# Kernel optimization log

Measured on AMD Instinct MI355X. Metric: run time of the kernel, lower is better.

## Reference

```python
import jax, jax.numpy as jnp
import numpy as np
import math

B, T, C, H = 4, 2048, 1024, 16
D = C // H  # head dim = 64

def setup_inputs() -> dict:
    key = jax.random.key(0)
    k1, k2, k3 = jax.random.split(key, 3)
    scale = 0.02
    return {
        "x": jax.random.normal(k1, (B, T, C), dtype=jnp.float32),
        "W_qkv": jax.random.normal(k2, (C, 3 * C), dtype=jnp.float32) * scale,
        "b_qkv": jnp.zeros((3 * C,), dtype=jnp.float32),
        "W_proj": jax.random.normal(k3, (C, C), dtype=jnp.float32) * scale,
        "b_proj": jnp.zeros((C,), dtype=jnp.float32),
    }

def reference(x, W_qkv, b_qkv, W_proj, b_proj):
    Bx, Tx, Cx = x.shape
    qkv = x @ W_qkv + b_qkv                      # [B, T, 3C]
    q, k, v = jnp.split(qkv, 3, axis=-1)
    # [B, T, C] -> [B, H, T, D]
    q = q.reshape(Bx, Tx, H, D).transpose(0, 2, 1, 3)
    k = k.reshape(Bx, Tx, H, D).transpose(0, 2, 1, 3)
    v = v.reshape(Bx, Tx, H, D).transpose(0, 2, 1, 3)
    scores = jnp.einsum("bhqd,bhkd->bhqk", q, k) * (1.0 / math.sqrt(D))
    causal = jnp.tril(jnp.ones((Tx, Tx), dtype=bool))  # [T, T]
    scores = jnp.where(causal[None, None, :, :], scores, jnp.finfo(scores.dtype).min)
    attn = jax.nn.softmax(scores, axis=-1)
    # dropout(p=0.1) in the original is stochastic; omitted for a deterministic baseline
    out = jnp.einsum("bhqk,bhkd->bhqd", attn, v)   # [B, H, T, D]
    out = out.transpose(0, 2, 1, 3).reshape(Bx, Tx, Cx)
    return out @ W_proj + b_proj
```

## Files before the change

kernel.cpp:

```cpp
#include <hip/hip_runtime.h>
#include <hip/hip_bf16.h>
#include <cstdint>
#include <cstddef>

#define Bsz 4
#define Tseq 2048
#define Cdim 1024
#define Hh 16
#define Dh 64

typedef unsigned short u16;
typedef __bf16 bfx8 __attribute__((ext_vector_type(8)));
typedef float f32x4 __attribute__((ext_vector_type(4)));
typedef float f32x16 __attribute__((ext_vector_type(16)));
typedef unsigned short u16x8 __attribute__((ext_vector_type(8)));

#define AS1 __attribute__((address_space(1)))
#define AS3 __attribute__((address_space(3)))

#define QSCALE 0.18033688f

__device__ __forceinline__ u16 f2b(float f) {
  union { float f; unsigned u; } x; x.f = f;
  unsigned r = x.u + 0x7FFFu + ((x.u >> 16) & 1u);
  return (u16)(r >> 16);
}
__device__ __forceinline__ float b2f(u16 b) {
  union { unsigned u; float f; } x; x.u = ((unsigned)b) << 16; return x.f;
}
__device__ __forceinline__ unsigned cvtpk(float lo, float hi) {
  unsigned r;
  asm("v_cvt_pk_bf16_f32 %0, %1, %2" : "=v"(r) : "v"(lo), "v"(hi));
  return r;
}
__device__ __forceinline__ void swap32(unsigned &a, unsigned &b) {
  asm("v_permlane32_swap_b32 %0, %1" : "+v"(a), "+v"(b));
}

__global__ __launch_bounds__(256) void cvt_f32_bf16(const float* __restrict__ in,
                                                    u16* __restrict__ out, int n4) {
  int i = blockIdx.x * 256 + threadIdx.x;
  if (i < n4) {
    const float4 v = reinterpret_cast<const float4*>(in)[i];
    ushort4 o;
    o.x = f2b(v.x); o.y = f2b(v.y); o.z = f2b(v.z); o.w = f2b(v.w);
    reinterpret_cast<ushort4*>(out)[i] = o;
  }
}

__global__ __launch_bounds__(256) void transpose_cvt(const float* __restrict__ in,
                                                     u16* __restrict__ out, int R, int Cn) {
  __shared__ float tile[32][33];
  const int c0 = blockIdx.x * 32, r0 = blockIdx.y * 32;
  const int tx = threadIdx.x, ty = threadIdx.y;
  for (int i = ty; i < 32; i += 8)
    tile[i][tx] = in[(size_t)(r0 + i) * Cn + c0 + tx];
  __syncthreads();
  for (int i = ty; i < 32; i += 8)
    out[(size_t)(c0 + i) * R + r0 + tx] = f2b(tile[tx][i]);
}

template<int MODE>
__global__ __launch_bounds__(512, 4) void gemm_bt(const u16* __restrict__ A, const u16* __restrict__ Bt,
                                                  const float* __restrict__ bias, void* __restrict__ Cout,
                                                  u16* __restrict__ vtout,
                                                  int M, int N, int K) {
  __shared__ __align__(16) u16 Alds[3][4096];
  __shared__ __align__(16) u16 Blds[3][8192];
  const int tid = threadIdx.x;
  const int lane = tid & 63;
  const int wid = tid >> 6;
  const int nwgx = gridDim.x;
  const int nwg = nwgx * gridDim.y;
  int lin = blockIdx.y * nwgx + blockIdx.x;
  lin = (lin & 7) * (nwg >> 3) + (lin >> 3);
  const int mbase = (lin / nwgx) * 128;
  const int nbase = (lin % nwgx) * 256;
  const int wm = wid & 1, wn = wid >> 1;

  const int sLlow = lane >> 3;
  const int s8 = (lane & 7) ^ sLlow;
  const int srow = 2 * (wid * 8 + sLlow) + (s8 >> 2);
  const int skof = (s8 & 3) * 8;

  const u16* pa  = A  + (size_t)(mbase + srow) * K + skof;
  const u16* pb0 = Bt + (size_t)(nbase + srow) * K + skof;
  const u16* pb1 = pb0 + (size_t)128 * K;

  const int raA = wm * 64 + (lane & 15);
  const int LA = raA >> 1;
  const int pA = ((raA & 1) * 4 + (lane >> 4)) ^ (LA & 7);
  const int aoffw = LA * 64 + pA * 8;
  const int rbB = wn * 64 + (lane & 15);
  const int LB = rbB >> 1;
  const int pB = ((rbB & 1) * 4 + (lane >> 4)) ^ (LB & 7);
  const int boffw = LB * 64 + pB * 8;

  AS3 u16* aldsb = (AS3 u16*)&Alds[0][0];
  AS3 u16* bldsb = (AS3 u16*)&Blds[0][0];

  const f32x4 vzero = {0.f, 0.f, 0.f, 0.f};
  f32x4 acc[4][4];
  #pragma unroll
  for (int i = 0; i < 4; ++i)
    #pragma unroll
    for (int j = 0; j < 4; ++j) acc[i][j] = vzero;

  const int NT = K >> 5;

  auto stage = [&](int slot) {
    __builtin_amdgcn_global_load_lds((AS1 void*)const_cast<u16*>(pa),
                                     (AS3 void*)&Alds[slot][wid * 512], 16, 0, 0);
    __builtin_amdgcn_global_load_lds((AS1 void*)const_cast<u16*>(pb0),
                                     (AS3 void*)&Blds[slot][wid * 512], 16, 0, 0);
    __builtin_amdgcn_global_load_lds((AS1 void*)const_cast<u16*>(pb1),
                                     (AS3 void*)&Blds[slot][4096 + wid * 512], 16, 0, 0);
    pa += 32; pb0 += 32; pb1 += 32;
  };

  stage(0);
  stage(1);
  asm volatile("s_waitcnt vmcnt(3)" ::: "memory");
  __builtin_amdgcn_s_barrier();

  int slot = 0, pf = 2;
  for (int t = 0; t < NT; ++t) {
    if (t + 2 < NT) stage(pf);

    bfx8 af[4], bfv[4];
    {
      AS3 u16* ap = aldsb + slot * 4096 + aoffw;
      AS3 u16* bp = bldsb + slot * 8192 + boffw;
      asm volatile("ds_read_b128 %0, %1"             : "=v"(af[0])  : "v"(ap));
      asm volatile("ds_read_b128 %0, %1 offset:1024" : "=v"(af[1])  : "v"(ap));
      asm volatile("ds_read_b128 %0, %1 offset:2048" : "=v"(af[2])  : "v"(ap));
      asm volatile("ds_read_b128 %0, %1 offset:3072" : "=v"(af[3])  : "v"(ap));
      asm volatile("ds_read_b128 %0, %1"             : "=v"(bfv[0]) : "v"(bp));
      asm volatile("ds_read_b128 %0, %1 offset:1024" : "=v"(bfv[1]) : "v"(bp));
      asm volatile("ds_read_b128 %0, %1 offset:2048" : "=v"(bfv[2]) : "v"(bp));
      asm volatile("ds_read_b128 %0, %1 offset:3072" : "=v"(bfv[3]) : "v"(bp));
    }
    asm volatile("s_waitcnt lgkmcnt(0)" ::: "memory");
    __builtin_amdgcn_sched_barrier(0);

    __builtin_amdgcn_s_setprio(1);
    #pragma unroll
    for (int mf = 0; mf < 4; ++mf)
      #pragma unroll
      for (int nf = 0; nf < 4; ++nf)
        acc[mf][nf] = __builtin_amdgcn_mfma_f32_16x16x32_bf16(af[mf], bfv[nf], acc[mf][nf], 0, 0, 0);
    __builtin_amdgcn_s_setprio(0);

    if (t + 2 < NT)      { asm volatile("s_waitcnt vmcnt(3)" ::: "memory"); }
    else if (t + 1 < NT) { asm volatile("s_waitcnt vmcnt(0)" ::: "memory"); }
    if (t + 1 < NT) __builtin_amdgcn_s_barrier();

    slot = (slot == 2) ? 0 : slot + 1;
    pf   = (pf == 2) ? 0 : pf + 1;
  }

  float bv[4];
  #pragma unroll
  for (int nf = 0; nf < 4; ++nf) bv[nf] = bias[nbase + wn * 64 + nf * 16 + (lane & 15)];
  #pragma unroll
  for (int mf = 0; mf < 4; ++mf) {
    #pragma unroll
    for (int nf = 0; nf < 4; ++nf) {
      const int r0 = mbase + wm * 64 + mf * 16 + (lane >> 4) * 4;
      const int c  = nbase + wn * 64 + nf * 16 + (lane & 15);
      const int cb = nbase + wn * 64 + nf * 16;
      const float cscale = (MODE == 1 && cb >= 1024 && cb < 2048) ? QSCALE : 1.0f;
      float v[4];
      #pragma unroll
      for (int j = 0; j < 4; ++j) v[j] = (acc[mf][nf][j] + bv[nf]) * cscale;
      if (MODE == 1 && cb >= 2048) {
        const int hh = (c - 2048) >> 6, dd = (c - 2048) & 63;
        const int bb = r0 >> 11, tt = r0 & 2047;
        ushort4 pkd;
        pkd.x = f2b(v[0]); pkd.y = f2b(v[1]); pkd.z = f2b(v[2]); pkd.w = f2b(v[3]);
        *reinterpret_cast<ushort4*>(
            &vtout[(((size_t)bb * Hh + hh) * Dh + dd) * Tseq + tt]) = pkd;
      } else {
        #pragma unroll
        for (int j = 0; j < 4; ++j) {
          if (MODE == 1) ((u16*)Cout)[(size_t)(r0 + j) * N + c] = f2b(v[j]);
          else           ((float*)Cout)[(size_t)(r0 + j) * N + c] = v[j];
        }
      }
    }
  }
}

#define ROWI(r) (((r) & 3) + 8 * ((r) >> 2))
__global__ __launch_bounds__(512, 4) void attn_fwd(const u16* __restrict__ qkv,
                                                   const u16* __restrict__ vt,
                                                   u16* __restrict__ aout) {
  __shared__ __align__(16) u16 Klds[4][64 * 64];
  __shared__ __align__(16) u16 Vtlds[4][64 * 64];
  const int tid = threadIdx.x;
  const int lane = tid & 63;
  const int wid = tid >> 6;
  const int qg = wid & 3;
  const int half = wid >> 2;
  const int lin = blockIdx.y * gridDim.x + blockIdx.x;
  const int bh = (lin & 7) * 8 + ((lin >> 3) & 7);
  const int qpair = lin >> 6;
  const int b = bh >> 4, h = bh & 15;
  const int hi4 = (lane & 32) >> 3;

  const int stg_row = lane >> 3;
  const int stg_srcslot = (lane & 7) ^ (stg_row & 7);

  const u16* gkbase = qkv + ((size_t)b * Tseq + wid * 8 + stg_row) * 3072
                      + 1024 + h * 64 + stg_srcslot * 8;
  const u16* gvbase = vt + ((size_t)bh * Dh + wid * 8 + stg_row) * Tseq + stg_srcslot * 8;

  float* Olds = reinterpret_cast<float*>(&Klds[0][0]);
  float* Llds = reinterpret_cast<float*>(&Vtlds[0][0]);

  #pragma unroll 1
  for (int pass = 0; pass < 2; ++pass) {
    const int qtile = pass ? qpair : (15 - qpair);
    const int qwb = qtile * 128 + qg * 32;
    const int ntiles = qtile * 2 + 2;

    bfx8 qf[4];
    {
      const int qrow = qwb + (lane & 31);
      #pragma unroll
      for (int c = 0; c < 4; ++c) {
        const u16* src = qkv + (size_t)(b * Tseq + qrow) * 3072 + h * 64 + c * 16 + (hi4 << 1);
        qf[c] = *reinterpret_cast<const bfx8*>(src);
      }
    }

    float l_r = 0.f;
    f32x16 o0, o1;
    #pragma unroll
    for (int r = 0; r < 16; ++r) { o0[r] = 0.f; o1[r] = 0.f; }

    auto stageT = [&](int t) {
      const u16* gk = gkbase + (size_t)t * 64 * 3072;
      const u16* gv = gvbase + t * 64;
      __builtin_amdgcn_global_load_lds((AS1 void*)const_cast<u16*>(gk),
                                       (AS3 void*)&Klds[t & 3][wid * 512], 16, 0, 0);
      __builtin_amdgcn_global_load_lds((AS1 void*)const_cast<u16*>(gv),
                                       (AS3 void*)&Vtlds[t & 3][wid * 512], 16, 0, 0);
    };
    stageT(0);
    stageT(1);
    __syncthreads();

    for (int t = 0; t < ntiles; t += 2) {
      if (t + 2 < ntiles) stageT(t + 2);
      if (t + 3 < ntiles) stageT(t + 3);

      const int tt = t + half;
      const int kb = tt * 64;
      const int buf = tt & 3;
      if (kb <= qwb + 31) {
        f32x16 st0, st1;
        #pragma unroll
        for (int r = 0; r < 16; ++r) { st0[r] = 0.f; st1[r] = 0.f; }
        __builtin_amdgcn_s_setprio(1);
        #pragma unroll
        for (int c = 0; c < 4; ++c) {
          const int row0 = lane & 31;
          const int sl = (c * 2 + (lane >> 5)) ^ (row0 & 7);
          const bfx8 k0 = *reinterpret_cast<const bfx8*>(&Klds[buf][row0 * 64 + sl * 8]);
          const bfx8 k1 = *reinterpret_cast<const bfx8*>(&Klds[buf][(row0 + 32) * 64 + sl * 8]);
          st0 = __builtin_amdgcn_mfma_f32_32x32x16_bf16(k0, qf[c], st0, 0, 0, 0);
          st1 = __builtin_amdgcn_mfma_f32_32x32x16_bf16(k1, qf[c], st1, 0, 0, 0);
        }
        __builtin_amdgcn_s_setprio(0);

        if (kb + 63 > qwb) {
          const int qg_ = qwb + (lane & 31);
          #pragma unroll
          for (int r = 0; r < 16; ++r) {
            const int kt = kb + ROWI(r) + hi4;
            if (kt > qg_) st0[r] = -1e30f;
            if (kt + 32 > qg_) st1[r] = -1e30f;
          }
        }

        float rs = 0.f;
        #pragma unroll
        for (int r = 0; r < 16; ++r) { st0[r] = exp2f(st0[r]); rs += st0[r]; }
        #pragma unroll
        for (int r = 0; r < 16; ++r) { st1[r] = exp2f(st1[r]); rs += st1[r]; }
        rs += __shfl_xor(rs, 32);
        l_r += rs;

        bfx8 pf[4];
        #pragma unroll
        for (int tph = 0; tph < 2; ++tph) {
          #pragma unroll
          for (int c2 = 0; c2 < 2; ++c2) {
            const int rb = c2 * 8;
            float s0 = tph ? st1[rb + 0] : st0[rb + 0], s1 = tph ? st1[rb + 1] : st0[rb + 1];
            float s2 = tph ? st1[rb + 2] : st0[rb + 2], s3 = tph ? st1[rb + 3] : st0[rb + 3];
            float s4 = tph ? st1[rb + 4] : st0[rb + 4], s5 = tph ? st1[rb + 5] : st0[rb + 5];
            float s6 = tph ? st1[rb + 6] : st0[rb + 6], s7 = tph ? st1[rb + 7] : st0[rb + 7];
            unsigned w0 = cvtpk(s0, s1);
            unsigned w2 = cvtpk(s4, s5);
            swap32(w0, w2);
            unsigned w1 = cvtpk(s2, s3);
            unsigned w3 = cvtpk(s6, s7);
            swap32(w1, w3);
            union { unsigned w[4]; bfx8 v; } u;
            u.w[0] = w0; u.w[1] = w1; u.w[2] = w2; u.w[3] = w3;
            pf[tph * 2 + c2] = u.v;
          }
        }

        __builtin_amdgcn_s_setprio(1);
        #pragma unroll
        for (int c4 = 0; c4 < 4; ++c4) {
          const int vrow = lane & 31;
          const int sl = (c4 * 2 + (lane >> 5)) ^ (vrow & 7);
          const bfx8 vf0 = *reinterpret_cast<const bfx8*>(&Vtlds[buf][vrow * 64 + sl * 8]);
          const bfx8 vf1 = *reinterpret_cast<const bfx8*>(&Vtlds[buf][(vrow + 32) * 64 + sl * 8]);
          o0 = __builtin_amdgcn_mfma_f32_32x32x16_bf16(pf[c4], vf0, o0, 0, 0, 0);
          o1 = __builtin_amdgcn_mfma_f32_32x32x16_bf16(pf[c4], vf1, o1, 0, 0, 0);
        }
        __builtin_amdgcn_s_setprio(0);
      }

      __syncthreads();
    }

    if (half == 1) {
      Llds[qg * 64 + lane] = l_r;
      #pragma unroll
      for (int r = 0; r < 16; ++r) {
        Olds[qg * 2048 + r * 64 + lane]        = o0[r];
        Olds[qg * 2048 + (r + 16) * 64 + lane] = o1[r];
      }
    }
    __syncthreads();
    if (half == 0) {
      const float l1 = Llds[qg * 64 + lane];
      const float linv = 1.0f / (l_r + l1);
      #pragma unroll
      for (int r = 0; r < 16; ++r) {
        const int src = ROWI(r) + hi4;
        const float cr = __shfl(linv, src);
        const int q = qwb + src;
        const float v0 = (o0[r] + Olds[qg * 2048 + r * 64 + lane]) * cr;
        const float v1 = (o1[r] + Olds[qg * 2048 + (r + 16) * 64 + lane]) * cr;
        aout[(size_t)(b * Tseq + q) * 1024 + h * 64 + (lane & 31)]      = f2b(v0);
        aout[(size_t)(b * Tseq + q) * 1024 + h * 64 + 32 + (lane & 31)] = f2b(v1);
      }
    }
    __syncthreads();
  }
}

extern "C" void kernel_launch(void* const* d_in, const int* in_sizes, int n_in,
                              void* d_out, int out_size, void* d_ws, size_t ws_size,
                              hipStream_t stream) {
  const float* x      = (const float*)d_in[0];
  const float* W_qkv  = (const float*)d_in[1];
  const float* b_qkv  = (const float*)d_in[2];
  const float* W_proj = (const float*)d_in[3];
  const float* b_proj = (const float*)d_in[4];
  float* out = (float*)d_out;

  char* ws = (char*)d_ws;
  const size_t SZ_XB    = 16777216;
  const size_t SZ_WQKV  = 6291456;
  const size_t SZ_WPROJ = 2097152;
  const size_t SZ_QKV   = 50331648;
  u16* xb     = (u16*)ws;
  u16* wqkvT  = (u16*)(ws + SZ_XB);
  u16* wprojT = (u16*)(ws + SZ_XB + SZ_WQKV);
  u16* qkv    = (u16*)(ws + SZ_XB + SZ_WQKV + SZ_WPROJ);
  u16* vt     = (u16*)(ws + SZ_XB + SZ_WQKV + SZ_WPROJ + SZ_QKV);

  cvt_f32_bf16<<<dim3((Bsz * Tseq * Cdim / 4 + 255) / 256), dim3(256), 0, stream>>>(
      x, xb, Bsz * Tseq * Cdim / 4);
  transpose_cvt<<<dim3(3 * Cdim / 32, Cdim / 32), dim3(32, 8), 0, stream>>>(W_qkv, wqkvT, Cdim, 3 * Cdim);
  transpose_cvt<<<dim3(Cdim / 32, Cdim / 32), dim3(32, 8), 0, stream>>>(W_proj, wprojT, Cdim, Cdim);
  gemm_bt<1><<<dim3(3 * Cdim / 256, Bsz * Tseq / 128), dim3(512), 0, stream>>>(
      xb, wqkvT, b_qkv, qkv, vt, Bsz * Tseq, 3 * Cdim, Cdim);
  attn_fwd<<<dim3(8, Bsz * Hh), dim3(512), 0, stream>>>(qkv, vt, xb);
  gemm_bt<0><<<dim3(Cdim / 256, Bsz * Tseq / 128), dim3(512), 0, stream>>>(
      xb, wprojT, b_proj, out, nullptr, Bsz * Tseq, Cdim, Cdim);
}
```

Baseline: 167.4 us.

## Restructure attention: one q-tile per block, split KV tile across halves, triple-buffer

Attention now launches one block per 128-row query tile instead of pairing tiles per block, with heaviest tiles scheduled first. Within a KV tile, the two wave halves each take 32 keys instead of whole alternating 64-key tiles. Staging moves to a 3-slot ring with one tile per iteration and vmcnt-based waits plus raw barriers, replacing the 4-slot, two-tiles-per-step scheme. It also uses v_exp_f32 directly and raises the occupancy hint to 6 blocks per CU, which may increase register pressure and adds more per-tile barriers.

```diff
diff --git a/kernel.cpp b/kernel.cpp
--- a/kernel.cpp
+++ b/kernel.cpp
@@ -35,6 +35,11 @@
 }
 __device__ __forceinline__ void swap32(unsigned &a, unsigned &b) {
   asm("v_permlane32_swap_b32 %0, %1" : "+v"(a), "+v"(b));
+}
+__device__ __forceinline__ float fexp2(float x) {
+  float r;
+  asm("v_exp_f32 %0, %1" : "=v"(r) : "v"(x));
+  return r;
 }
 
 __global__ __launch_bounds__(256) void cvt_f32_bf16(const float* __restrict__ in,
@@ -192,168 +197,154 @@
 }
 
 #define ROWI(r) (((r) & 3) + 8 * ((r) >> 2))
-__global__ __launch_bounds__(512, 4) void attn_fwd(const u16* __restrict__ qkv,
+__global__ __launch_bounds__(512, 6) void attn_fwd(const u16* __restrict__ qkv,
                                                    const u16* __restrict__ vt,
                                                    u16* __restrict__ aout) {
-  __shared__ __align__(16) u16 Klds[4][64 * 64];
-  __shared__ __align__(16) u16 Vtlds[4][64 * 64];
+  __shared__ __align__(16) u16 SMEM[2][3][4096];
   const int tid = threadIdx.x;
   const int lane = tid & 63;
   const int wid = tid >> 6;
   const int qg = wid & 3;
   const int half = wid >> 2;
-  const int lin = blockIdx.y * gridDim.x + blockIdx.x;
-  const int bh = (lin & 7) * 8 + ((lin >> 3) & 7);
-  const int qpair = lin >> 6;
+  const int bh = ((blockIdx.y & 7) << 3) | (blockIdx.y >> 3);
+  const int qtile = 15 - (int)blockIdx.x;
   const int b = bh >> 4, h = bh & 15;
   const int hi4 = (lane & 32) >> 3;
 
-  const int stg_row = lane >> 3;
-  const int stg_srcslot = (lane & 7) ^ (stg_row & 7);
-
-  const u16* gkbase = qkv + ((size_t)b * Tseq + wid * 8 + stg_row) * 3072
-                      + 1024 + h * 64 + stg_srcslot * 8;
-  const u16* gvbase = vt + ((size_t)bh * Dh + wid * 8 + stg_row) * Tseq + stg_srcslot * 8;
-
-  float* Olds = reinterpret_cast<float*>(&Klds[0][0]);
-  float* Llds = reinterpret_cast<float*>(&Vtlds[0][0]);
-
-  #pragma unroll 1
-  for (int pass = 0; pass < 2; ++pass) {
-    const int qtile = pass ? qpair : (15 - qpair);
-    const int qwb = qtile * 128 + qg * 32;
-    const int ntiles = qtile * 2 + 2;
-
-    bfx8 qf[4];
-    {
-      const int qrow = qwb + (lane & 31);
+  const int stg_row = tid >> 3;
+  const int stg_slot = (tid & 7) ^ (stg_row & 7);
+  const u16* gk0 = qkv + ((size_t)b * Tseq + stg_row) * 3072 + 1024 + h * 64 + stg_slot * 8;
+  const u16* gv0 = vt + ((size_t)bh * Dh + stg_row) * Tseq + stg_slot * 8;
+  AS3 u16* kdst = (AS3 u16*)&SMEM[0][0][wid * 512];
+  AS3 u16* vdst = (AS3 u16*)&SMEM[1][0][wid * 512];
+
+  const int qwb = qtile * 128 + qg * 32;
+  const int ntiles = qtile * 2 + 2;
+
+  bfx8 qf[4];
+  {
+    const int qrow = qwb + (lane & 31);
+    #pragma unroll
+    for (int c = 0; c < 4; ++c) {
+      const u16* src = qkv + (size_t)(b * Tseq + qrow) * 3072 + h * 64 + c * 16 + (hi4 << 1);
+      qf[c] = *reinterpret_cast<const bfx8*>(src);
+    }
+  }
+
+  float l_r = 0.f;
+  f32x16 o0, o1;
+  #pragma unroll
+  for (int r = 0; r < 16; ++r) { o0[r] = 0.f; o1[r] = 0.f; }
+
+  auto stageT = [&](int t, int slot) {
+    __builtin_amdgcn_global_load_lds((AS1 void*)const_cast<u16*>(gk0 + (size_t)t * 64 * 3072),
+                                     (AS3 void*)(kdst + slot * 4096), 16, 0, 0);
+    __builtin_amdgcn_global_load_lds((AS1 void*)const_cast<u16*>(gv0 + t * 64),
+                                     (AS3 void*)(vdst + slot * 4096), 16, 0, 0);
+  };
+  stageT(0, 0);
+  stageT(1, 1);
+  asm volatile("s_waitcnt vmcnt(2)" ::: "memory");
+  __builtin_amdgcn_s_barrier();
+
+  int buf = 0, sbuf = 2;
+  const int khb = half * 32;
+  for (int t = 0; t < ntiles; ++t) {
+    if (t + 2 < ntiles) stageT(t + 2, sbuf);
+    const int kb = t * 64 + khb;
+    if (kb <= qwb + 31) {
+      const u16* Kb = &SMEM[0][buf][0];
+      const u16* Vb = &SMEM[1][buf][0];
+      f32x16 st;
+      #pragma unroll
+      for (int r = 0; r < 16; ++r) st[r] = 0.f;
+      const int row0 = khb + (lane & 31);
+      __builtin_amdgcn_s_setprio(1);
       #pragma unroll
       for (int c = 0; c < 4; ++c) {
-        const u16* src = qkv + (size_t)(b * Tseq + qrow) * 3072 + h * 64 + c * 16 + (hi4 << 1);
-        qf[c] = *reinterpret_cast<const bfx8*>(src);
-      }
-    }
-
-    float l_r = 0.f;
-    f32x16 o0, o1;
-    #pragma unroll
-    for (int r = 0; r < 16; ++r) { o0[r] = 0.f; o1[r] = 0.f; }
-
-    auto stageT = [&](int t) {
-      const u16* gk = gkbase + (size_t)t * 64 * 3072;
-      const u16* gv = gvbase + t * 64;
-      __builtin_amdgcn_global_load_lds((AS1 void*)const_cast<u16*>(gk),
-                                       (AS3 void*)&Klds[t & 3][wid * 512], 16, 0, 0);
-      __builtin_amdgcn_global_load_lds((AS1 void*)const_cast<u16*>(gv),
-                                       (AS3 void*)&Vtlds[t & 3][wid * 512], 16, 0, 0);
-    };
-    stageT(0);
-    stageT(1);
-    __syncthreads();
-
-    for (int t = 0; t < ntiles; t += 2) {
-      if (t + 2 < ntiles) stageT(t + 2);
-      if (t + 3 < ntiles) stageT(t + 3);
-
-      const int tt = t + half;
-      const int kb = tt * 64;
-      const int buf = tt & 3;
-      if (kb <= qwb + 31) {
-        f32x16 st0, st1;
+        const int sl = (c * 2 + (lane >> 5)) ^ (row0 & 7);
+        const bfx8 k0 = *reinterpret_cast<const bfx8*>(&Kb[row0 * 64 + sl * 8]);
+        st = __builtin_amdgcn_mfma_f32_32x32x16_bf16(k0, qf[c], st, 0, 0, 0);
+      }
+      __builtin_amdgcn_s_setprio(0);
+
+      if (kb + 31 > qwb) {
+        const int q_ = qwb + (lane & 31);
         #pragma unroll
-        for (int r = 0; r < 16; ++r) { st0[r] = 0.f; st1[r] = 0.f; }
-        __builtin_amdgcn_s_setprio(1);
-        #pragma unroll
-        for (int c = 0; c < 4; ++c) {
-          const int row0 = lane & 31;
-          const int sl = (c * 2 + (lane >> 5)) ^ (row0 & 7);
-          const bfx8 k0 = *reinterpret_cast<const bfx8*>(&Klds[buf][row0 * 64 + sl * 8]);
-          const bfx8 k1 = *reinterpret_cast<const bfx8*>(&Klds[buf][(row0 + 32) * 64 + sl * 8]);
-          st0 = __builtin_amdgcn_mfma_f32_32x32x16_bf16(k0, qf[c], st0, 0, 0, 0);
-          st1 = __builtin_amdgcn_mfma_f32_32x32x16_bf16(k1, qf[c], st1, 0, 0, 0);
+        for (int r = 0; r < 16; ++r) {
+          if (kb + ROWI(r) + hi4 > q_) st[r] = -1e30f;
         }
-        __builtin_amdgcn_s_setprio(0);
-
-        if (kb + 63 > qwb) {
-          const int qg_ = qwb + (lane & 31);
-          #pragma unroll
-          for (int r = 0; r < 16; ++r) {
-            const int kt = kb + ROWI(r) + hi4;
-            if (kt > qg_) st0[r] = -1e30f;
-            if (kt + 32 > qg_) st1[r] = -1e30f;
-          }
-        }
-
-        float rs = 0.f;
-        #pragma unroll
-        for (int r = 0; r < 16; ++r) { st0[r] = exp2f(st0[r]); rs += st0[r]; }
-        #pragma unroll
-        for (int r = 0; r < 16; ++r) { st1[r] = exp2f(st1[r]); rs += st1[r]; }
-        rs += __shfl_xor(rs, 32);
-        l_r += rs;
-
-        bfx8 pf[4];
-        #pragma unroll
-        for (int tph = 0; tph < 2; ++tph) {
-          #pragma unroll
-          for (int c2 = 0; c2 < 2; ++c2) {
-            const int rb = c2 * 8;
-            float s0 = tph ? st1[rb + 0] : st0[rb + 0], s1 = tph ? st1[rb + 1] : st0[rb + 1];
-            float s2 = tph ? st1[rb + 2] : st0[rb + 2], s3 = tph ? st1[rb + 3] : st0[rb + 3];
-            float s4 = tph ? st1[rb + 4] : st0[rb + 4], s5 = tph ? st1[rb + 5] : st0[rb + 5];
-            float s6 = tph ? st1[rb + 6] : st0[rb + 6], s7 = tph ? st1[rb + 7] : st0[rb + 7];
-            unsigned w0 = cvtpk(s0, s1);
-            unsigned w2 = cvtpk(s4, s5);
-            swap32(w0, w2);
-            unsigned w1 = cvtpk(s2, s3);
-            unsigned w3 = cvtpk(s6, s7);
-            swap32(w1, w3);
-            union { unsigned w[4]; bfx8 v; } u;
-            u.w[0] = w0; u.w[1] = w1; u.w[2] = w2; u.w[3] = w3;
-            pf[tph * 2 + c2] = u.v;
-          }
-        }
-
-        __builtin_amdgcn_s_setprio(1);
-        #pragma unroll
-        for (int c4 = 0; c4 < 4; ++c4) {
-          const int vrow = lane & 31;
-          const int sl = (c4 * 2 + (lane >> 5)) ^ (vrow & 7);
-          const bfx8 vf0 = *reinterpret_cast<const bfx8*>(&Vtlds[buf][vrow * 64 + sl * 8]);
-          const bfx8 vf1 = *reinterpret_cast<const bfx8*>(&Vtlds[buf][(vrow + 32) * 64 + sl * 8]);
-          o0 = __builtin_amdgcn_mfma_f32_32x32x16_bf16(pf[c4], vf0, o0, 0, 0, 0);
-          o1 = __builtin_amdgcn_mfma_f32_32x32x16_bf16(pf[c4], vf1, o1, 0, 0, 0);
-        }
-        __builtin_amdgcn_s_setprio(0);
-      }
-
-      __syncthreads();
-    }
-
-    if (half == 1) {
-      Llds[qg * 64 + lane] = l_r;
-      #pragma unroll
-      for (int r = 0; r < 16; ++r) {
-        Olds[qg * 2048 + r * 64 + lane]        = o0[r];
-        Olds[qg * 2048 + (r + 16) * 64 + lane] = o1[r];
-      }
-    }
-    __syncthreads();
-    if (half == 0) {
-      const float l1 = Llds[qg * 64 + lane];
-      const float linv = 1.0f / (l_r + l1);
-      #pragma unroll
-      for (int r = 0; r < 16; ++r) {
-        const int src = ROWI(r) + hi4;
-        const float cr = __shfl(linv, src);
-        const int q = qwb + src;
-        const float v0 = (o0[r] + Olds[qg * 2048 + r * 64 + lane]) * cr;
-        const float v1 = (o1[r] + Olds[qg * 2048 + (r + 16) * 64 + lane]) * cr;
-        aout[(size_t)(b * Tseq + q) * 1024 + h * 64 + (lane & 31)]      = f2b(v0);
-        aout[(size_t)(b * Tseq + q) * 1024 + h * 64 + 32 + (lane & 31)] = f2b(v1);
-      }
-    }
-    __syncthreads();
+      }
+
+      float rs = 0.f;
+      #pragma unroll
+      for (int r = 0; r < 16; ++r) { st[r] = fexp2(st[r]); rs += st[r]; }
+      rs += __shfl_xor(rs, 32);
+      l_r += rs;
+
+      bfx8 pfr[2];
+      #pragma unroll
+      for (int c2 = 0; c2 < 2; ++c2) {
+        const int rb = c2 * 8;
+        unsigned w0 = cvtpk(st[rb + 0], st[rb + 1]);
+        unsigned w2 = cvtpk(st[rb + 4], st[rb + 5]);
+        swap32(w0, w2);
+        unsigned w1 = cvtpk(st[rb + 2], st[rb + 3]);
+        unsigned w3 = cvtpk(st[rb + 6], st[rb + 7]);
+        swap32(w1, w3);
+        union { unsigned w[4]; bfx8 v; } u;
+        u.w[0] = w0; u.w[1] = w1; u.w[2] = w2; u.w[3] = w3;
+        pfr[c2] = u.v;
+      }
+
+      const int vrow = lane & 31;
+      __builtin_amdgcn_s_setprio(1);
+      #pragma unroll
+      for (int c4 = 0; c4 < 2; ++c4) {
+        const int sl = (half * 4 + c4 * 2 + (lane >> 5)) ^ (vrow & 7);
+        const bfx8 vf0 = *reinterpret_cast<const bfx8*>(&Vb[vrow * 64 + sl * 8]);
+        const bfx8 vf1 = *reinterpret_cast<const bfx8*>(&Vb[(vrow + 32) * 64 + sl * 8]);
+        o0 = __builtin_amdgcn_mfma_f32_32x32x16_bf16(pfr[c4], vf0, o0, 0, 0, 0);
+        o1 = __builtin_amdgcn_mfma_f32_32x32x16_bf16(pfr[c4], vf1, o1, 0, 0, 0);
+      }
+      __builtin_amdgcn_s_setprio(0);
+    }
+
+    if (t + 1 < ntiles) {
+      if (t + 2 < ntiles) { asm volatile("s_waitcnt vmcnt(2)" ::: "memory"); }
+      else                { asm volatile("s_waitcnt vmcnt(0)" ::: "memory"); }
+      __builtin_amdgcn_s_barrier();
+    }
+    buf  = (buf == 2) ? 0 : buf + 1;
+    sbuf = (sbuf == 2) ? 0 : sbuf + 1;
+  }
+
+  __syncthreads();
+
+  float* Olds = reinterpret_cast<float*>(&SMEM[0][0][0]);
+  float* Llds = Olds + 8192;
+  if (half == 1) {
+    Llds[qg * 64 + lane] = l_r;
+    #pragma unroll
+    for (int r = 0; r < 16; ++r) {
+      Olds[qg * 2048 + r * 64 + lane]        = o0[r];
+      Olds[qg * 2048 + (r + 16) * 64 + lane] = o1[r];
+    }
+  }
+  __syncthreads();
+  if (half == 0) {
+    const float l1 = Llds[qg * 64 + lane];
+    const float linv = 1.0f / (l_r + l1);
+    #pragma unroll
+    for (int r = 0; r < 16; ++r) {
+      const int src = ROWI(r) + hi4;
+      const float cr = __shfl(linv, src);
+      const int q = qwb + src;
+      const float v0 = (o0[r] + Olds[qg * 2048 + r * 64 + lane]) * cr;
+      const float v1 = (o1[r] + Olds[qg * 2048 + (r + 16) * 64 + lane]) * cr;
+      aout[(size_t)(b * Tseq + q) * 1024 + h * 64 + (lane & 31)]      = f2b(v0);
+      aout[(size_t)(b * Tseq + q) * 1024 + h * 64 + 32 + (lane & 31)] = f2b(v1);
+    }
   }
 }
 
@@ -384,7 +375,7 @@
   transpose_cvt<<<dim3(Cdim / 32, Cdim / 32), dim3(32, 8), 0, stream>>>(W_proj, wprojT, Cdim, Cdim);
   gemm_bt<1><<<dim3(3 * Cdim / 256, Bsz * Tseq / 128), dim3(512), 0, stream>>>(
       xb, wqkvT, b_qkv, qkv, vt, Bsz * Tseq, 3 * Cdim, Cdim);
-  attn_fwd<<<dim3(8, Bsz * Hh), dim3(512), 0, stream>>>(qkv, vt, xb);
+  attn_fwd<<<dim3(16, 64), dim3(512), 0, stream>>>(qkv, vt, xb);
   gemm_bt<0><<<dim3(Cdim / 256, Bsz * Tseq / 128), dim3(512), 0, stream>>>(
       xb, wprojT, b_proj, out, nullptr, Bsz * Tseq, Cdim, Cdim);
 }
```

Measured after the change: 269.8 us. 61.2% more time.

## Shrink GEMM tile to 128x128 and software-pipeline LDS reads with MFMAs

Applied to the files above, without the earlier changes.

The GEMM block tile shrinks from 128x256 with 512 threads to 128x128 with 256 threads, and launch bounds change to (256,3). The B LDS buffer shrinks accordingly and each thread now issues four global-to-LDS loads per stage. The main loop is restructured into double-buffered register fragments: the next tile's ds_reads are issued between the two halves of the current tile's MFMAs, so LDS latency overlaps matrix math. This doubles the grid size and trades per-block reuse for more blocks and better latency hiding.

```diff
diff --git a/kernel.cpp b/kernel.cpp
--- a/kernel.cpp
+++ b/kernel.cpp
@@ -60,13 +60,22 @@
     out[(size_t)(c0 + i) * R + r0 + tx] = f2b(tile[tx][i]);
 }
 
+#define MFMA_HALF(afS, bfS, MLO)                                                              \
+  _Pragma("unroll")                                                                           \
+  for (int nf = 0; nf < 4; ++nf) {                                                            \
+    acc[(MLO)][nf] = __builtin_amdgcn_mfma_f32_16x16x32_bf16(afS[(MLO)], bfS[nf],             \
+                                                             acc[(MLO)][nf], 0, 0, 0);       \
+    acc[(MLO) + 1][nf] = __builtin_amdgcn_mfma_f32_16x16x32_bf16(afS[(MLO) + 1], bfS[nf],     \
+                                                                 acc[(MLO) + 1][nf], 0, 0, 0);\
+  }
+
 template<int MODE>
-__global__ __launch_bounds__(512, 4) void gemm_bt(const u16* __restrict__ A, const u16* __restrict__ Bt,
+__global__ __launch_bounds__(256, 3) void gemm_bt(const u16* __restrict__ A, const u16* __restrict__ Bt,
                                                   const float* __restrict__ bias, void* __restrict__ Cout,
                                                   u16* __restrict__ vtout,
                                                   int M, int N, int K) {
   __shared__ __align__(16) u16 Alds[3][4096];
-  __shared__ __align__(16) u16 Blds[3][8192];
+  __shared__ __align__(16) u16 Blds[3][4096];
   const int tid = threadIdx.x;
   const int lane = tid & 63;
   const int wid = tid >> 6;
@@ -75,17 +84,18 @@
   int lin = blockIdx.y * nwgx + blockIdx.x;
   lin = (lin & 7) * (nwg >> 3) + (lin >> 3);
   const int mbase = (lin / nwgx) * 128;
-  const int nbase = (lin % nwgx) * 256;
+  const int nbase = (lin % nwgx) * 128;
   const int wm = wid & 1, wn = wid >> 1;
 
-  const int sLlow = lane >> 3;
-  const int s8 = (lane & 7) ^ sLlow;
-  const int srow = 2 * (wid * 8 + sLlow) + (s8 >> 2);
+  const int sL = tid >> 3;
+  const int s8 = (tid & 7) ^ (sL & 7);
+  const int srow = 2 * sL + (s8 >> 2);
   const int skof = (s8 & 3) * 8;
 
-  const u16* pa  = A  + (size_t)(mbase + srow) * K + skof;
+  const u16* pa0 = A  + (size_t)(mbase + srow) * K + skof;
+  const u16* pa1 = pa0 + (size_t)64 * K;
   const u16* pb0 = Bt + (size_t)(nbase + srow) * K + skof;
-  const u16* pb1 = pb0 + (size_t)128 * K;
+  const u16* pb1 = pb0 + (size_t)64 * K;
 
   const int raA = wm * 64 + (lane & 15);
   const int LA = raA >> 1;
@@ -109,54 +119,62 @@
   const int NT = K >> 5;
 
   auto stage = [&](int slot) {
-    __builtin_amdgcn_global_load_lds((AS1 void*)const_cast<u16*>(pa),
-                                     (AS3 void*)&Alds[slot][wid * 512], 16, 0, 0);
+    __builtin_amdgcn_global_load_lds((AS1 void*)const_cast<u16*>(pa0),
+                                     (AS3 void*)&Alds[slot][tid * 8], 16, 0, 0);
+    __builtin_amdgcn_global_load_lds((AS1 void*)const_cast<u16*>(pa1),
+                                     (AS3 void*)&Alds[slot][2048 + tid * 8], 16, 0, 0);
     __builtin_amdgcn_global_load_lds((AS1 void*)const_cast<u16*>(pb0),
-                                     (AS3 void*)&Blds[slot][wid * 512], 16, 0, 0);
+                                     (AS3 void*)&Blds[slot][tid * 8], 16, 0, 0);
     __builtin_amdgcn_global_load_lds((AS1 void*)const_cast<u16*>(pb1),
-                                     (AS3 void*)&Blds[slot][4096 + wid * 512], 16, 0, 0);
-    pa += 32; pb0 += 32; pb1 += 32;
+                                     (AS3 void*)&Blds[slot][2048 + tid * 8], 16, 0, 0);
+    pa0 += 32; pa1 += 32; pb0 += 32; pb1 += 32;
+  };
+
+  bfx8 afA[4], bfA[4], afB[4], bfB[4];
+  auto dsread = [&](int slot, bfx8* afD, bfx8* bfD) {
+    AS3 u16* ap = aldsb + slot * 4096 + aoffw;
+    AS3 u16* bp = bldsb + slot * 4096 + boffw;
+    asm volatile("ds_read_b128 %0, %1"             : "=v"(afD[0]) : "v"(ap));
+    asm volatile("ds_read_b128 %0, %1 offset:1024" : "=v"(afD[1]) : "v"(ap));
+    asm volatile("ds_read_b128 %0, %1 offset:2048" : "=v"(afD[2]) : "v"(ap));
+    asm volatile("ds_read_b128 %0, %1 offset:3072" : "=v"(afD[3]) : "v"(ap));
+    asm volatile("ds_read_b128 %0, %1"             : "=v"(bfD[0]) : "v"(bp));
+    asm volatile("ds_read_b128 %0, %1 offset:1024" : "=v"(bfD[1]) : "v"(bp));
+    asm volatile("ds_read_b128 %0, %1 offset:2048" : "=v"(bfD[2]) : "v"(bp));
+    asm volatile("ds_read_b128 %0, %1 offset:3072" : "=v"(bfD[3]) : "v"(bp));
+  };
+
+  int pf = 2, rs = 1;
+  auto subiter = [&](int t, bfx8* afC, bfx8* bfC, bfx8* afN, bfx8* bfN) {
+    if (t + 2 < NT) { stage(pf); pf = (pf == 2) ? 0 : pf + 1; }
+    __builtin_amdgcn_s_setprio(1);
+    MFMA_HALF(afC, bfC, 0);
+    __builtin_amdgcn_s_setprio(0);
+    if (t + 1 < NT) {
+      if (t + 2 < NT) { asm volatile("s_waitcnt vmcnt(4)" ::: "memory"); }
+      else            { asm volatile("s_waitcnt vmcnt(0)" ::: "memory"); }
+      __builtin_amdgcn_s_barrier();
+      dsread(rs, afN, bfN);
+      rs = (rs == 2) ? 0 : rs + 1;
+    }
+    __builtin_amdgcn_s_setprio(1);
+    MFMA_HALF(afC, bfC, 2);
+    __builtin_amdgcn_s_setprio(0);
+    asm volatile("s_waitcnt lgkmcnt(0)" ::: "memory");
+    __builtin_amdgcn_sched_barrier(0);
   };
 
   stage(0);
   stage(1);
-  asm volatile("s_waitcnt vmcnt(3)" ::: "memory");
+  asm volatile("s_waitcnt vmcnt(4)" ::: "memory");
   __builtin_amdgcn_s_barrier();
-
-  int slot = 0, pf = 2;
-  for (int t = 0; t < NT; ++t) {
-    if (t + 2 < NT) stage(pf);
-
-    bfx8 af[4], bfv[4];
-    {
-      AS3 u16* ap = aldsb + slot * 4096 + aoffw;
-      AS3 u16* bp = bldsb + slot * 8192 + boffw;
-      asm volatile("ds_read_b128 %0, %1"             : "=v"(af[0])  : "v"(ap));
-      asm volatile("ds_read_b128 %0, %1 offset:1024" : "=v"(af[1])  : "v"(ap));
-      asm volatile("ds_read_b128 %0, %1 offset:2048" : "=v"(af[2])  : "v"(ap));
-      asm volatile("ds_read_b128 %0, %1 offset:3072" : "=v"(af[3])  : "v"(ap));
-      asm volatile("ds_read_b128 %0, %1"             : "=v"(bfv[0]) : "v"(bp));
-      asm volatile("ds_read_b128 %0, %1 offset:1024" : "=v"(bfv[1]) : "v"(bp));
-      asm volatile("ds_read_b128 %0, %1 offset:2048" : "=v"(bfv[2]) : "v"(bp));
-      asm volatile("ds_read_b128 %0, %1 offset:3072" : "=v"(bfv[3]) : "v"(bp));
-    }
-    asm volatile("s_waitcnt lgkmcnt(0)" ::: "memory");
-    __builtin_amdgcn_sched_barrier(0);
-
-    __builtin_amdgcn_s_setprio(1);
-    #pragma unroll
-    for (int mf = 0; mf < 4; ++mf)
-      #pragma unroll
-      for (int nf = 0; nf < 4; ++nf)
-        acc[mf][nf] = __builtin_amdgcn_mfma_f32_16x16x32_bf16(af[mf], bfv[nf], acc[mf][nf], 0, 0, 0);
-    __builtin_amdgcn_s_setprio(0);
-
-    if (t + 2 < NT)      { asm volatile("s_waitcnt vmcnt(3)" ::: "memory"); }
-    else if (t + 1 < NT) { asm volatile("s_waitcnt vmcnt(0)" ::: "memory"); }
-    if (t + 1 < NT) __builtin_amdgcn_s_barrier();
-
-    slot = (slot == 2) ? 0 : slot + 1;
-    pf   = (pf == 2) ? 0 : pf + 1;
+  dsread(0, afA, bfA);
+  asm volatile("s_waitcnt lgkmcnt(0)" ::: "memory");
+  __builtin_amdgcn_sched_barrier(0);
+
+  for (int t = 0; t < NT; t += 2) {
+    subiter(t,     afA, bfA, afB, bfB);
+    subiter(t + 1, afB, bfB, afA, bfA);
   }
 
   float bv[4];
@@ -382,9 +400,9 @@
       x, xb, Bsz * Tseq * Cdim / 4);
   transpose_cvt<<<dim3(3 * Cdim / 32, Cdim / 32), dim3(32, 8), 0, stream>>>(W_qkv, wqkvT, Cdim, 3 * Cdim);
   transpose_cvt<<<dim3(Cdim / 32, Cdim / 32), dim3(32, 8), 0, stream>>>(W_proj, wprojT, Cdim, Cdim);
-  gemm_bt<1><<<dim3(3 * Cdim / 256, Bsz * Tseq / 128), dim3(512), 0, stream>>>(
+  gemm_bt<1><<<dim3(3 * Cdim / 128, Bsz * Tseq / 128), dim3(256), 0, stream>>>(
       xb, wqkvT, b_qkv, qkv, vt, Bsz * Tseq, 3 * Cdim, Cdim);
   attn_fwd<<<dim3(8, Bsz * Hh), dim3(512), 0, stream>>>(qkv, vt, xb);
-  gemm_bt<0><<<dim3(Cdim / 256, Bsz * Tseq / 128), dim3(512), 0, stream>>>(
+  gemm_bt<0><<<dim3(Cdim / 128, Bsz * Tseq / 128), dim3(256), 0, stream>>>(
       xb, wprojT, b_proj, out, nullptr, Bsz * Tseq, Cdim, Cdim);
 }
```

Result: slower. 173.2 us (+3.5%).

## Deepen K prefetch with a five-slot ring and fine-grained vmcnt waits

Applied to the files above, without the earlier changes.

K tiles now go into a five-slot LDS ring, so the next pair's K loads can be issued a full iteration ahead, while V stays in a four-slot ring. The per-iteration __syncthreads is replaced by s_waitcnt vmcnt(1) plus s_barrier, which lets the most recent load stay in flight across the barrier, with the V stage for t+4 issued after the barrier. The aim is to hide global-to-LDS latency better and avoid draining all outstanding loads at every step. The cost is extra LDS use (one more 8 KB K buffer), which may reduce occupancy, and more fragile hand-written wait-count ordering.

```diff
diff --git a/kernel.cpp b/kernel.cpp
--- a/kernel.cpp
+++ b/kernel.cpp
@@ -195,8 +195,8 @@
 __global__ __launch_bounds__(512, 4) void attn_fwd(const u16* __restrict__ qkv,
                                                    const u16* __restrict__ vt,
                                                    u16* __restrict__ aout) {
-  __shared__ __align__(16) u16 Klds[4][64 * 64];
-  __shared__ __align__(16) u16 Vtlds[4][64 * 64];
+  __shared__ __align__(16) u16 Klds[5][4096];
+  __shared__ __align__(16) u16 Vtlds[4][4096];
   const int tid = threadIdx.x;
   const int lane = tid & 63;
   const int wid = tid >> 6;
@@ -239,25 +239,41 @@
     #pragma unroll
     for (int r = 0; r < 16; ++r) { o0[r] = 0.f; o1[r] = 0.f; }
 
-    auto stageT = [&](int t) {
-      const u16* gk = gkbase + (size_t)t * 64 * 3072;
-      const u16* gv = gvbase + t * 64;
-      __builtin_amdgcn_global_load_lds((AS1 void*)const_cast<u16*>(gk),
-                                       (AS3 void*)&Klds[t & 3][wid * 512], 16, 0, 0);
-      __builtin_amdgcn_global_load_lds((AS1 void*)const_cast<u16*>(gv),
-                                       (AS3 void*)&Vtlds[t & 3][wid * 512], 16, 0, 0);
+    auto stageK = [&](int t, int slot) {
+      __builtin_amdgcn_global_load_lds((AS1 void*)const_cast<u16*>(gkbase + (size_t)t * 64 * 3072),
+                                       (AS3 void*)&Klds[slot][wid * 512], 16, 0, 0);
     };
-    stageT(0);
-    stageT(1);
-    __syncthreads();
-
+    auto stageV = [&](int t, int slot) {
+      __builtin_amdgcn_global_load_lds((AS1 void*)const_cast<u16*>(gvbase + t * 64),
+                                       (AS3 void*)&Vtlds[slot][wid * 512], 16, 0, 0);
+    };
+
+    stageK(0, 0); stageV(0, 0);
+    stageK(1, 1); stageV(1, 1);
+    if (2 < ntiles) {
+      stageK(2, 2);
+      asm volatile("s_waitcnt vmcnt(1)" ::: "memory");
+      __builtin_amdgcn_s_barrier();
+      stageV(2, 2);
+    } else {
+      asm volatile("s_waitcnt vmcnt(0)" ::: "memory");
+      __builtin_amdgcn_s_barrier();
+    }
+
+    int s0 = 0;
     for (int t = 0; t < ntiles; t += 2) {
-      if (t + 2 < ntiles) stageT(t + 2);
-      if (t + 3 < ntiles) stageT(t + 3);
+      int sl3 = s0 + 3; if (sl3 >= 5) sl3 -= 5;
+      int sl4 = s0 + 4; if (sl4 >= 5) sl4 -= 5;
+      if (t + 3 < ntiles) {
+        stageK(t + 3, sl3);
+        stageV(t + 3, (t + 3) & 3);
+        if (t + 4 < ntiles) stageK(t + 4, sl4);
+      }
 
       const int tt = t + half;
       const int kb = tt * 64;
-      const int buf = tt & 3;
+      int kbuf = s0 + half; if (kbuf >= 5) kbuf -= 5;
+      const int vbuf = tt & 3;
       if (kb <= qwb + 31) {
         f32x16 st0, st1;
         #pragma unroll
@@ -267,8 +283,8 @@
         for (int c = 0; c < 4; ++c) {
           const int row0 = lane & 31;
           const int sl = (c * 2 + (lane >> 5)) ^ (row0 & 7);
-          const bfx8 k0 = *reinterpret_cast<const bfx8*>(&Klds[buf][row0 * 64 + sl * 8]);
-          const bfx8 k1 = *reinterpret_cast<const bfx8*>(&Klds[buf][(row0 + 32) * 64 + sl * 8]);
+          const bfx8 k0 = *reinterpret_cast<const bfx8*>(&Klds[kbuf][row0 * 64 + sl * 8]);
+          const bfx8 k1 = *reinterpret_cast<const bfx8*>(&Klds[kbuf][(row0 + 32) * 64 + sl * 8]);
           st0 = __builtin_amdgcn_mfma_f32_32x32x16_bf16(k0, qf[c], st0, 0, 0, 0);
           st1 = __builtin_amdgcn_mfma_f32_32x32x16_bf16(k1, qf[c], st1, 0, 0, 0);
         }
@@ -298,15 +314,15 @@
           #pragma unroll
           for (int c2 = 0; c2 < 2; ++c2) {
             const int rb = c2 * 8;
-            float s0 = tph ? st1[rb + 0] : st0[rb + 0], s1 = tph ? st1[rb + 1] : st0[rb + 1];
-            float s2 = tph ? st1[rb + 2] : st0[rb + 2], s3 = tph ? st1[rb + 3] : st0[rb + 3];
-            float s4 = tph ? st1[rb + 4] : st0[rb + 4], s5 = tph ? st1[rb + 5] : st0[rb + 5];
-            float s6 = tph ? st1[rb + 6] : st0[rb + 6], s7 = tph ? st1[rb + 7] : st0[rb + 7];
-            unsigned w0 = cvtpk(s0, s1);
-            unsigned w2 = cvtpk(s4, s5);
+            float s0v = tph ? st1[rb + 0] : st0[rb + 0], s1v = tph ? st1[rb + 1] : st0[rb + 1];
+            float s2v = tph ? st1[rb + 2] : st0[rb + 2], s3v = tph ? st1[rb + 3] : st0[rb + 3];
+            float s4v = tph ? st1[rb + 4] : st0[rb + 4], s5v = tph ? st1[rb + 5] : st0[rb + 5];
+            float s6v = tph ? st1[rb + 6] : st0[rb + 6], s7v = tph ? st1[rb + 7] : st0[rb + 7];
+            unsigned w0 = cvtpk(s0v, s1v);
+            unsigned w2 = cvtpk(s4v, s5v);
             swap32(w0, w2);
-            unsigned w1 = cvtpk(s2, s3);
-            unsigned w3 = cvtpk(s6, s7);
+            unsigned w1 = cvtpk(s2v, s3v);
+            unsigned w3 = cvtpk(s6v, s7v);
             swap32(w1, w3);
             union { unsigned w[4]; bfx8 v; } u;
             u.w[0] = w0; u.w[1] = w1; u.w[2] = w2; u.w[3] = w3;
@@ -319,16 +335,26 @@
         for (int c4 = 0; c4 < 4; ++c4) {
           const int vrow = lane & 31;
           const int sl = (c4 * 2 + (lane >> 5)) ^ (vrow & 7);
-          const bfx8 vf0 = *reinterpret_cast<const bfx8*>(&Vtlds[buf][vrow * 64 + sl * 8]);
-          const bfx8 vf1 = *reinterpret_cast<const bfx8*>(&Vtlds[buf][(vrow + 32) * 64 + sl * 8]);
+          const bfx8 vf0 = *reinterpret_cast<const bfx8*>(&Vtlds[vbuf][vrow * 64 + sl * 8]);
+          const bfx8 vf1 = *reinterpret_cast<const bfx8*>(&Vtlds[vbuf][(vrow + 32) * 64 + sl * 8]);
           o0 = __builtin_amdgcn_mfma_f32_32x32x16_bf16(pf[c4], vf0, o0, 0, 0, 0);
           o1 = __builtin_amdgcn_mfma_f32_32x32x16_bf16(pf[c4], vf1, o1, 0, 0, 0);
         }
         __builtin_amdgcn_s_setprio(0);
       }
 
-      __syncthreads();
-    }
+      if (t + 4 < ntiles) {
+        asm volatile("s_waitcnt vmcnt(1)" ::: "memory");
+        __builtin_amdgcn_s_barrier();
+        stageV(t + 4, (t + 4) & 3);
+      } else if (t + 2 < ntiles) {
+        asm volatile("s_waitcnt vmcnt(0)" ::: "memory");
+        __builtin_amdgcn_s_barrier();
+      }
+      s0 += 2; if (s0 >= 5) s0 -= 5;
+    }
+
+    __syncthreads();
 
     if (half == 1) {
       Llds[qg * 64 + lane] = l_r;
```

Result: slower. 171.9 us (+2.7%).
